# Optimization experiments

Measured on AMD Instinct MI355X. Metric: run time of the kernel, lower is better.

Reference implementation:

```python
import jax, jax.numpy as jnp
import numpy as np

B, S, DIM, H = 8, 1024, 1024, 16
D = DIM // H  # d_head = 64


def setup_inputs() -> dict:
    key = jax.random.key(0)
    ks = jax.random.split(key, 7)
    scale = 1.0 / np.sqrt(D)  # nn.Linear default init range ~ U(-1/sqrt(in), 1/sqrt(in))
    x = jax.random.normal(ks[0], (B, S, DIM), dtype=jnp.float32)
    Wq = jax.random.uniform(ks[1], (H, D, D), jnp.float32, -scale, scale)
    Wk = jax.random.uniform(ks[2], (H, D, D), jnp.float32, -scale, scale)
    Wv = jax.random.uniform(ks[3], (H, D, D), jnp.float32, -scale, scale)
    bq = jax.random.uniform(ks[4], (H, D), jnp.float32, -scale, scale)
    bk = jax.random.uniform(ks[5], (H, D), jnp.float32, -scale, scale)
    bv = jax.random.uniform(ks[6], (H, D), jnp.float32, -scale, scale)
    return {"x": x, "Wq": Wq, "Wk": Wk, "Wv": Wv, "bq": bq, "bk": bk, "bv": bv}


def reference(x, Wq, Wk, Wv, bq, bk, bv):
    # x: [B,S,DIM] -> split heads: [B,S,H,D] (matches per-head column slicing)
    xh = x.reshape(x.shape[0], x.shape[1], H, D)
    # per-head linear: y = x @ W.T + b  (nn.Linear convention: weight [out,in])
    q = jnp.einsum('bshd,hed->bshe', xh, Wq) + bq  # [B,S,H,D]
    k = jnp.einsum('bshd,hed->bshe', xh, Wk) + bk
    v = jnp.einsum('bshd,hed->bshe', xh, Wv) + bv
    scores = jnp.einsum('bqhd,bkhd->bhqk', q, k) / jnp.sqrt(jnp.float32(D))
    attn = jax.nn.softmax(scores, axis=-1)  # [B,H,S,S]
    out = jnp.einsum('bhqk,bkhd->bqhd', attn, v)  # [B,S,H,D]
    # hstack over heads == merge last two dims back to DIM
    return out.reshape(x.shape[0], x.shape[1], H * D)
```

## Files before the change

kernel.cpp:

```cpp
#include <hip/hip_runtime.h>
#include <hip/hip_bf16.h>

#define BB 8
#define SS 1024
#define HH 16
#define DD 64
#define DIMM 1024
#define NUNITS (BB * HH)
#define UNIT_ELEMS (SS * DD)

typedef __attribute__((ext_vector_type(8))) short short8;
typedef __attribute__((ext_vector_type(4))) float f32x4;

#if __has_builtin(__builtin_amdgcn_exp2f)
#define EXP2F(x) __builtin_amdgcn_exp2f(x)
#else
#define EXP2F(x) exp2f(x)
#endif
#if __has_builtin(__builtin_amdgcn_rcpf)
#define RCPF(x) __builtin_amdgcn_rcpf(x)
#else
#define RCPF(x) (1.0f / (x))
#endif

__device__ inline short f2b(float f) {
    unsigned u = __float_as_uint(f);
    u = (u + 0x7FFFu + ((u >> 16) & 1u)) >> 16;
    return (short)u;
}
__device__ inline unsigned pk2(float lo, float hi) {
    unsigned a = __float_as_uint(lo), b = __float_as_uint(hi);
    a = (a + 0x7FFFu + ((a >> 16) & 1u)) >> 16;
    b = (b + 0x7FFFu + ((b >> 16) & 1u)) & 0xFFFF0000u;
    return a | b;
}

__global__ __launch_bounds__(256) void qkv_proj(
    const float* __restrict__ x, const float* __restrict__ Wq,
    const float* __restrict__ Wk, const float* __restrict__ Wv,
    const float* __restrict__ bqp, const float* __restrict__ bkp,
    const float* __restrict__ bvp,
    short* __restrict__ Qo, short* __restrict__ Ko, short* __restrict__ Vto,
    int unit0)
{
    __shared__ alignas(16) short wsm[3][64][72];
    __shared__ alignas(16) short xs[64][72];
    __shared__ alignas(16) short tr[64][72];

    const int t = threadIdx.x;
    const int bid = blockIdx.x;
    const int stg = bid & 3;
    const int ul = bid >> 2;
    const int unit = unit0 + ul;
    const int h = unit & 15;
    const int b = unit >> 4;

    for (int m = 0; m < 3; ++m) {
        const float* src = ((m == 0) ? Wq : (m == 1) ? Wk : Wv) + h * DD * DD;
        for (int i = 0; i < 4; ++i) {
            int g = t + i * 256;
            int e = g >> 4, c = (g & 15) * 4;
            float4 wv = *reinterpret_cast<const float4*>(src + e * DD + c);
            short4 sv; sv.x = f2b(wv.x); sv.y = f2b(wv.y); sv.z = f2b(wv.z); sv.w = f2b(wv.w);
            *reinterpret_cast<short4*>(&wsm[m][e][c]) = sv;
        }
    }

    const int lane = t & 63, w = t >> 6;
    const int l15 = lane & 15, quad = lane >> 4;

    for (int st2 = 0; st2 < 4; ++st2) {
        const int s0 = (stg * 4 + st2) * 64;
        if (st2) __syncthreads();
        for (int i = 0; i < 4; ++i) {
            int g = t + i * 256;
            int r = g >> 4, c = (g & 15) * 4;
            float4 xv = *reinterpret_cast<const float4*>(
                x + ((size_t)(b * SS + s0 + r)) * DIMM + h * DD + c);
            short4 sv; sv.x = f2b(xv.x); sv.y = f2b(xv.y); sv.z = f2b(xv.z); sv.w = f2b(xv.w);
            *reinterpret_cast<short4*>(&xs[r][c]) = sv;
        }
        __syncthreads();

        short8 a0 = *reinterpret_cast<const short8*>(&xs[w * 16 + l15][quad * 8]);
        short8 a1 = *reinterpret_cast<const short8*>(&xs[w * 16 + l15][32 + quad * 8]);

        f32x4 acc[12];
        for (int m = 0; m < 3; ++m)
            for (int et = 0; et < 4; ++et) {
                short8 w0 = *reinterpret_cast<const short8*>(&wsm[m][et * 16 + l15][quad * 8]);
                short8 w1 = *reinterpret_cast<const short8*>(&wsm[m][et * 16 + l15][32 + quad * 8]);
                f32x4 a = {0.f, 0.f, 0.f, 0.f};
                a = __builtin_amdgcn_mfma_f32_16x16x32_bf16(a0, w0, a, 0, 0, 0);
                a = __builtin_amdgcn_mfma_f32_16x16x32_bf16(a1, w1, a, 0, 0, 0);
                acc[m * 4 + et] = a;
            }

        for (int m = 0; m < 3; ++m) {
            if (m) __syncthreads();
            const float* bp = (m == 0) ? bqp : (m == 1) ? bkp : bvp;
            const float scale = (m == 0) ? 0.125f : 1.0f;
            for (int et = 0; et < 4; ++et) {
                float bias = bp[h * DD + et * 16 + l15];
                int e = et * 16 + l15;
                for (int r = 0; r < 4; ++r) {
                    float v = (acc[m * 4 + et][r] + bias) * scale;
                    int srow = w * 16 + quad * 4 + r;
                    if (m == 2) tr[e][srow] = f2b(v);
                    else        tr[srow][e] = f2b(v);
                }
            }
            __syncthreads();
            for (int i = 0; i < 2; ++i) {
                int g = t + i * 256;
                int row = g >> 3, col = (g & 7) * 8;
                short8 val = *reinterpret_cast<const short8*>(&tr[row][col]);
                if (m == 0)
                    *reinterpret_cast<short8*>(Qo + ((size_t)ul * SS + s0 + row) * DD + col) = val;
                else if (m == 1)
                    *reinterpret_cast<short8*>(Ko + ((size_t)ul * SS + s0 + row) * DD + col) = val;
                else
                    *reinterpret_cast<short8*>(Vto + ((size_t)ul * DD + row) * SS + s0 + col) = val;
            }
        }
    }
}

__global__ __launch_bounds__(256, 4) void attn(
    const short* __restrict__ Q, const short* __restrict__ K,
    const short* __restrict__ Vt, float* __restrict__ out, int unit0, int nu)
{
    __shared__ alignas(16) short ks[64][72];
    __shared__ alignas(16) short vts[64][72];
    __shared__ alignas(16) short ps[4][32][72];

    const int t = threadIdx.x;
    const int bid = blockIdx.x;
    int ul, qt;
    if (nu == NUNITS) {
        int xslot = bid & 7;
        int j = bid >> 3;
        ul = xslot * 16 + (j & 15);
        qt = j >> 4;
    } else {
        ul = bid >> 3;
        qt = bid & 7;
    }
    const int unit = unit0 + ul;
    const int h = unit & 15;
    const int b = unit >> 4;
    const int q0 = qt * 128;
    const int lane = t & 63, w = t >> 6;
    const int l15 = lane & 15, quad = lane >> 4;

    short8 qa[2][2];
    for (int s = 0; s < 2; ++s) {
        const short* qp = Q + ((size_t)ul * SS + q0 + s * 64 + w * 16 + l15) * DD;
        qa[s][0] = *reinterpret_cast<const short8*>(qp + quad * 8);
        qa[s][1] = *reinterpret_cast<const short8*>(qp + 32 + quad * 8);
    }

    short8 ones;
    for (int j = 0; j < 8; ++j) ones[j] = (short)0x3F80;

    f32x4 o[8];
    f32x4 lacc[2];
    for (int i = 0; i < 8; ++i) o[i] = (f32x4){0.f, 0.f, 0.f, 0.f};
    lacc[0] = (f32x4){0.f, 0.f, 0.f, 0.f};
    lacc[1] = (f32x4){0.f, 0.f, 0.f, 0.f};

    const int srow_ = t >> 3, scol = (t & 7) * 8;

    const short* kg = K + (size_t)ul * UNIT_ELEMS + srow_ * DD + scol;
    const short* vg = Vt + (size_t)ul * UNIT_ELEMS + srow_ * SS + scol;
    char* ksw = (char*)&ks[srow_][scol];
    char* vtw = (char*)&vts[srow_][scol];
    const char* kbp = (const char*)&ks[l15][quad * 8];
    const char* vbp = (const char*)&vts[l15][quad * 8];
    const char* pap = (const char*)&ps[w][l15][quad * 8];
    char* psw = (char*)&ps[w][l15][quad * 4];

    const float L2E = 1.44269504f;
    const float MBIAS = 11.5415603f;

    for (int kt = 0; kt < 16; ++kt) {
        __syncthreads();
        *reinterpret_cast<short8*>(ksw) = *reinterpret_cast<const short8*>(kg);
        *reinterpret_cast<short8*>(ksw + 32 * 144) = *reinterpret_cast<const short8*>(kg + 32 * DD);
        *reinterpret_cast<short8*>(vtw) = *reinterpret_cast<const short8*>(vg);
        *reinterpret_cast<short8*>(vtw + 32 * 144) = *reinterpret_cast<const short8*>(vg + 32 * SS);
        kg += 64 * DD;
        vg += 64;
        __syncthreads();

        for (int n = 0; n < 4; ++n) {
            short8 kb0 = *reinterpret_cast<const short8*>(kbp + n * 2304);
            short8 kb1 = *reinterpret_cast<const short8*>(kbp + n * 2304 + 64);
            for (int s = 0; s < 2; ++s) {
                f32x4 a = {0.f, 0.f, 0.f, 0.f};
                a = __builtin_amdgcn_mfma_f32_16x16x32_bf16(kb0, qa[s][0], a, 0, 0, 0);
                a = __builtin_amdgcn_mfma_f32_16x16x32_bf16(kb1, qa[s][1], a, 0, 0, 0);
                float p0 = EXP2F(fmaf(a[0], L2E, -MBIAS));
                float p1 = EXP2F(fmaf(a[1], L2E, -MBIAS));
                float p2 = EXP2F(fmaf(a[2], L2E, -MBIAS));
                float p3 = EXP2F(fmaf(a[3], L2E, -MBIAS));
                uint2 pk; pk.x = pk2(p0, p1); pk.y = pk2(p2, p3);
                *reinterpret_cast<uint2*>(psw + s * 2304 + n * 32) = pk;
            }
        }

        short8 pa[2][2];
        for (int s = 0; s < 2; ++s) {
            pa[s][0] = *reinterpret_cast<const short8*>(pap + s * 2304);
            pa[s][1] = *reinterpret_cast<const short8*>(pap + s * 2304 + 64);
            lacc[s] = __builtin_amdgcn_mfma_f32_16x16x32_bf16(pa[s][0], ones, lacc[s], 0, 0, 0);
            lacc[s] = __builtin_amdgcn_mfma_f32_16x16x32_bf16(pa[s][1], ones, lacc[s], 0, 0, 0);
        }
        for (int dt = 0; dt < 4; ++dt) {
            short8 vb0 = *reinterpret_cast<const short8*>(vbp + dt * 2304);
            short8 vb1 = *reinterpret_cast<const short8*>(vbp + dt * 2304 + 64);
            for (int s = 0; s < 2; ++s) {
                o[s * 4 + dt] = __builtin_amdgcn_mfma_f32_16x16x32_bf16(pa[s][0], vb0, o[s * 4 + dt], 0, 0, 0);
                o[s * 4 + dt] = __builtin_amdgcn_mfma_f32_16x16x32_bf16(pa[s][1], vb1, o[s * 4 + dt], 0, 0, 0);
            }
        }
    }

    float* outp = out + ((size_t)b * SS + q0 + w * 16 + quad * 4) * DIMM + h * DD + l15;
    for (int s = 0; s < 2; ++s)
        for (int r = 0; r < 4; ++r) {
            float rin = RCPF(lacc[s][r]);
            for (int dt = 0; dt < 4; ++dt)
                outp[(size_t)(s * 64 + r) * DIMM + dt * 16] = o[s * 4 + dt][r] * rin;
        }
}

extern "C" void kernel_launch(void* const* d_in, const int* in_sizes, int n_in,
                              void* d_out, int out_size, void* d_ws, size_t ws_size,
                              hipStream_t stream) {
    const float* x   = (const float*)d_in[0];
    const float* Wq  = (const float*)d_in[1];
    const float* Wk  = (const float*)d_in[2];
    const float* Wv  = (const float*)d_in[3];
    const float* bqp = (const float*)d_in[4];
    const float* bkp = (const float*)d_in[5];
    const float* bvp = (const float*)d_in[6];
    float* out = (float*)d_out;

    const size_t unit_bytes = 3ULL * UNIT_ELEMS * sizeof(short);
    int U = (int)(ws_size / unit_bytes);
    if (U < 1) U = 1;
    if (U > NUNITS) U = NUNITS;

    short* Qw  = (short*)d_ws;
    short* Kw  = Qw + (size_t)U * UNIT_ELEMS;
    short* Vtw = Kw + (size_t)U * UNIT_ELEMS;

    for (int u0 = 0; u0 < NUNITS; u0 += U) {
        int nu = NUNITS - u0 < U ? NUNITS - u0 : U;
        qkv_proj<<<dim3(nu * 4), dim3(256), 0, stream>>>(
            x, Wq, Wk, Wv, bqp, bkp, bvp, Qw, Kw, Vtw, u0);
        attn<<<dim3(nu * 8), dim3(256), 0, stream>>>(Qw, Kw, Vtw, out, u0, nu);
    }
}
```

Baseline: 154.1 us.

## Rewrite attention inner loop with 32x32 MFMA, async LDS double-buffering, register P

Restructures the attention kernel around 32x32x16 MFMAs computing S^T so the exponentiated probabilities stay in registers. They are converted with v_cvt_pk_bf16 and exchanged across half-waves with permlane32_swap, so the per-wave LDS staging of P is gone. K and V tiles are loaded with global_load_lds into double-buffered, XOR-swizzled LDS, which removes one barrier per iteration and overlaps the next tile's load with compute. Row sums move from ones-MFMAs to VALU adds, and s_setprio is raised around the MFMA blocks. The risks are higher register pressure from the f32x16 accumulators, and correctness now depends on the swizzle and the lane permutation mapping.

Result: faster. 149.2 us (-3.2%).

```diff
diff --git a/kernel.cpp b/kernel.cpp
--- a/kernel.cpp
+++ b/kernel.cpp
@@ -11,6 +11,9 @@
 
 typedef __attribute__((ext_vector_type(8))) short short8;
 typedef __attribute__((ext_vector_type(4))) float f32x4;
+typedef __attribute__((ext_vector_type(16))) float f32x16;
+typedef __attribute__((ext_vector_type(2))) unsigned u32x2;
+typedef __attribute__((ext_vector_type(4))) unsigned u32x4;
 
 #if __has_builtin(__builtin_amdgcn_exp2f)
 #define EXP2F(x) __builtin_amdgcn_exp2f(x)
@@ -28,11 +31,18 @@
     u = (u + 0x7FFFu + ((u >> 16) & 1u)) >> 16;
     return (short)u;
 }
-__device__ inline unsigned pk2(float lo, float hi) {
-    unsigned a = __float_as_uint(lo), b = __float_as_uint(hi);
-    a = (a + 0x7FFFu + ((a >> 16) & 1u)) >> 16;
-    b = (b + 0x7FFFu + ((b >> 16) & 1u)) & 0xFFFF0000u;
-    return a | b;
+
+__device__ __forceinline__ unsigned cvtpk_bf16(float lo, float hi) {
+    unsigned r;
+    asm("v_cvt_pk_bf16_f32 %0, %1, %2" : "=v"(r) : "v"(lo), "v"(hi));
+    return r;
+}
+
+__device__ __forceinline__ void gll16(const void* g, void* l) {
+    __builtin_amdgcn_global_load_lds(
+        (const __attribute__((address_space(1))) void*)g,
+        (__attribute__((address_space(3))) void*)l,
+        16, 0, 0);
 }
 
 __global__ __launch_bounds__(256) void qkv_proj(
@@ -130,9 +140,9 @@
     const short* __restrict__ Q, const short* __restrict__ K,
     const short* __restrict__ Vt, float* __restrict__ out, int unit0, int nu)
 {
-    __shared__ alignas(16) short ks[64][72];
-    __shared__ alignas(16) short vts[64][72];
-    __shared__ alignas(16) short ps[4][32][72];
+    __shared__ alignas(16) short ksm[2][64][64];
+    __shared__ alignas(16) short vsm[2][64][64];
+    __shared__ float lsm[4][32];
 
     const int t = threadIdx.x;
     const int bid = blockIdx.x;
@@ -151,88 +161,124 @@
     const int b = unit >> 4;
     const int q0 = qt * 128;
     const int lane = t & 63, w = t >> 6;
-    const int l15 = lane & 15, quad = lane >> 4;
-
-    short8 qa[2][2];
-    for (int s = 0; s < 2; ++s) {
-        const short* qp = Q + ((size_t)ul * SS + q0 + s * 64 + w * 16 + l15) * DD;
-        qa[s][0] = *reinterpret_cast<const short8*>(qp + quad * 8);
-        qa[s][1] = *reinterpret_cast<const short8*>(qp + 32 + quad * 8);
-    }
-
-    short8 ones;
-    for (int j = 0; j < 8; ++j) ones[j] = (short)0x3F80;
-
-    f32x4 o[8];
-    f32x4 lacc[2];
-    for (int i = 0; i < 8; ++i) o[i] = (f32x4){0.f, 0.f, 0.f, 0.f};
-    lacc[0] = (f32x4){0.f, 0.f, 0.f, 0.f};
-    lacc[1] = (f32x4){0.f, 0.f, 0.f, 0.f};
-
-    const int srow_ = t >> 3, scol = (t & 7) * 8;
-
-    const short* kg = K + (size_t)ul * UNIT_ELEMS + srow_ * DD + scol;
-    const short* vg = Vt + (size_t)ul * UNIT_ELEMS + srow_ * SS + scol;
-    char* ksw = (char*)&ks[srow_][scol];
-    char* vtw = (char*)&vts[srow_][scol];
-    const char* kbp = (const char*)&ks[l15][quad * 8];
-    const char* vbp = (const char*)&vts[l15][quad * 8];
-    const char* pap = (const char*)&ps[w][l15][quad * 8];
-    char* psw = (char*)&ps[w][l15][quad * 4];
+    const int r5 = lane & 31;
+    const int hi = lane >> 5;
+    const int l7 = lane & 7;
+    const int hl4 = (hi ^ l7) << 4;
+
+    short8 qb[4];
+    {
+        const short* qp = Q + ((size_t)ul * SS + q0 + w * 32 + r5) * DD + hi * 8;
+#pragma unroll
+        for (int ds = 0; ds < 4; ++ds)
+            qb[ds] = *reinterpret_cast<const short8*>(qp + ds * 16);
+    }
+
+    const int lrow = lane >> 3, lch = (lane & 7) ^ lrow;
+    const short* kg = K + (size_t)ul * UNIT_ELEMS + (size_t)(w * 8 + lrow) * DD + lch * 8;
+    const short* vg = Vt + ((size_t)ul * DD + w * 8 + lrow) * SS + lch * 8;
+
+    const char* kread0 = (const char*)&ksm[0][0][0] + r5 * 128;
+    const char* vread0 = (const char*)&vsm[0][0][0] + r5 * 128;
+
+    f32x16 o0, o1;
+#pragma unroll
+    for (int i = 0; i < 16; ++i) { o0[i] = 0.f; o1[i] = 0.f; }
+    float lsum = 0.f;
 
     const float L2E = 1.44269504f;
     const float MBIAS = 11.5415603f;
 
+    {
+        short* lk = &ksm[0][w * 8][0];
+        short* lv = &vsm[0][w * 8][0];
+        gll16(kg, lk); gll16(kg + 32 * DD, lk + 32 * 64);
+        gll16(vg, lv); gll16(vg + 32 * SS, lv + 32 * 64);
+        kg += 64 * DD; vg += 64;
+    }
+
     for (int kt = 0; kt < 16; ++kt) {
+        const int cur = kt & 1;
         __syncthreads();
-        *reinterpret_cast<short8*>(ksw) = *reinterpret_cast<const short8*>(kg);
-        *reinterpret_cast<short8*>(ksw + 32 * 144) = *reinterpret_cast<const short8*>(kg + 32 * DD);
-        *reinterpret_cast<short8*>(vtw) = *reinterpret_cast<const short8*>(vg);
-        *reinterpret_cast<short8*>(vtw + 32 * 144) = *reinterpret_cast<const short8*>(vg + 32 * SS);
-        kg += 64 * DD;
-        vg += 64;
-        __syncthreads();
-
-        for (int n = 0; n < 4; ++n) {
-            short8 kb0 = *reinterpret_cast<const short8*>(kbp + n * 2304);
-            short8 kb1 = *reinterpret_cast<const short8*>(kbp + n * 2304 + 64);
-            for (int s = 0; s < 2; ++s) {
-                f32x4 a = {0.f, 0.f, 0.f, 0.f};
-                a = __builtin_amdgcn_mfma_f32_16x16x32_bf16(kb0, qa[s][0], a, 0, 0, 0);
-                a = __builtin_amdgcn_mfma_f32_16x16x32_bf16(kb1, qa[s][1], a, 0, 0, 0);
-                float p0 = EXP2F(fmaf(a[0], L2E, -MBIAS));
-                float p1 = EXP2F(fmaf(a[1], L2E, -MBIAS));
-                float p2 = EXP2F(fmaf(a[2], L2E, -MBIAS));
-                float p3 = EXP2F(fmaf(a[3], L2E, -MBIAS));
-                uint2 pk; pk.x = pk2(p0, p1); pk.y = pk2(p2, p3);
-                *reinterpret_cast<uint2*>(psw + s * 2304 + n * 32) = pk;
+
+        if (kt < 15) {
+            const int nxt = cur ^ 1;
+            short* lk = &ksm[nxt][w * 8][0];
+            short* lv = &vsm[nxt][w * 8][0];
+            gll16(kg, lk); gll16(kg + 32 * DD, lk + 32 * 64);
+            gll16(vg, lv); gll16(vg + 32 * SS, lv + 32 * 64);
+            kg += 64 * DD; vg += 64;
+        }
+
+        const char* kb_ = kread0 + cur * 8192;
+        const char* vb_ = vread0 + cur * 8192;
+
+        f32x16 c0, c1;
+#pragma unroll
+        for (int i = 0; i < 16; ++i) { c0[i] = 0.f; c1[i] = 0.f; }
+
+        __builtin_amdgcn_s_setprio(1);
+#pragma unroll
+        for (int ds = 0; ds < 4; ++ds) {
+            short8 ka = *reinterpret_cast<const short8*>(kb_ + ((ds << 5) ^ hl4));
+            short8 kb = *reinterpret_cast<const short8*>(kb_ + 4096 + ((ds << 5) ^ hl4));
+            c0 = __builtin_amdgcn_mfma_f32_32x32x16_bf16(ka, qb[ds], c0, 0, 0, 0);
+            c1 = __builtin_amdgcn_mfma_f32_32x32x16_bf16(kb, qb[ds], c1, 0, 0, 0);
+        }
+        __builtin_amdgcn_s_setprio(0);
+
+#pragma unroll
+        for (int n = 0; n < 2; ++n) {
+            f32x16 c = n ? c1 : c0;
+            float p[16];
+#pragma unroll
+            for (int r = 0; r < 16; ++r)
+                p[r] = EXP2F(fmaf(c[r], L2E, -MBIAS));
+            lsum += ((((p[0] + p[1]) + (p[2] + p[3])) + ((p[4] + p[5]) + (p[6] + p[7])))
+                   + (((p[8] + p[9]) + (p[10] + p[11])) + ((p[12] + p[13]) + (p[14] + p[15]))));
+
+#pragma unroll
+            for (int bb2 = 0; bb2 < 2; ++bb2) {
+                unsigned u0 = cvtpk_bf16(p[8 * bb2 + 0], p[8 * bb2 + 1]);
+                unsigned u1 = cvtpk_bf16(p[8 * bb2 + 2], p[8 * bb2 + 3]);
+                unsigned v0 = cvtpk_bf16(p[8 * bb2 + 4], p[8 * bb2 + 5]);
+                unsigned v1 = cvtpk_bf16(p[8 * bb2 + 6], p[8 * bb2 + 7]);
+                unsigned w0, w1c, w2, w3;
+#if __has_builtin(__builtin_amdgcn_permlane32_swap)
+                u32x2 r0 = __builtin_amdgcn_permlane32_swap(u0, v0, false, false);
+                u32x2 r1 = __builtin_amdgcn_permlane32_swap(u1, v1, false, false);
+                w0 = r0[0]; w2 = r0[1]; w1c = r1[0]; w3 = r1[1];
+#else
+                unsigned u0s = __shfl_xor(u0, 32), v0s = __shfl_xor(v0, 32);
+                unsigned u1s = __shfl_xor(u1, 32), v1s = __shfl_xor(v1, 32);
+                w0 = hi ? v0s : u0;  w2 = hi ? v0 : u0s;
+                w1c = hi ? v1s : u1; w3 = hi ? v1 : u1s;
+#endif
+                u32x4 aw; aw[0] = w0; aw[1] = w1c; aw[2] = w2; aw[3] = w3;
+                short8 af = __builtin_bit_cast(short8, aw);
+
+                const int ks = n * 2 + bb2;
+                short8 va = *reinterpret_cast<const short8*>(vb_ + ((ks << 5) ^ hl4));
+                short8 vb2 = *reinterpret_cast<const short8*>(vb_ + 4096 + ((ks << 5) ^ hl4));
+                __builtin_amdgcn_s_setprio(1);
+                o0 = __builtin_amdgcn_mfma_f32_32x32x16_bf16(af, va, o0, 0, 0, 0);
+                o1 = __builtin_amdgcn_mfma_f32_32x32x16_bf16(af, vb2, o1, 0, 0, 0);
+                __builtin_amdgcn_s_setprio(0);
             }
         }
-
-        short8 pa[2][2];
-        for (int s = 0; s < 2; ++s) {
-            pa[s][0] = *reinterpret_cast<const short8*>(pap + s * 2304);
-            pa[s][1] = *reinterpret_cast<const short8*>(pap + s * 2304 + 64);
-            lacc[s] = __builtin_amdgcn_mfma_f32_16x16x32_bf16(pa[s][0], ones, lacc[s], 0, 0, 0);
-            lacc[s] = __builtin_amdgcn_mfma_f32_16x16x32_bf16(pa[s][1], ones, lacc[s], 0, 0, 0);
-        }
-        for (int dt = 0; dt < 4; ++dt) {
-            short8 vb0 = *reinterpret_cast<const short8*>(vbp + dt * 2304);
-            short8 vb1 = *reinterpret_cast<const short8*>(vbp + dt * 2304 + 64);
-            for (int s = 0; s < 2; ++s) {
-                o[s * 4 + dt] = __builtin_amdgcn_mfma_f32_16x16x32_bf16(pa[s][0], vb0, o[s * 4 + dt], 0, 0, 0);
-                o[s * 4 + dt] = __builtin_amdgcn_mfma_f32_16x16x32_bf16(pa[s][1], vb1, o[s * 4 + dt], 0, 0, 0);
-            }
-        }
-    }
-
-    float* outp = out + ((size_t)b * SS + q0 + w * 16 + quad * 4) * DIMM + h * DD + l15;
-    for (int s = 0; s < 2; ++s)
-        for (int r = 0; r < 4; ++r) {
-            float rin = RCPF(lacc[s][r]);
-            for (int dt = 0; dt < 4; ++dt)
-                outp[(size_t)(s * 64 + r) * DIMM + dt * 16] = o[s * 4 + dt][r] * rin;
-        }
+    }
+
+    float lt = lsum + __shfl_xor(lsum, 32);
+    if (lane < 32) lsm[w][lane] = lt;
+
+#pragma unroll
+    for (int reg = 0; reg < 16; ++reg) {
+        const int row = (reg & 3) + 8 * (reg >> 2) + 4 * hi;
+        float rin = RCPF(lsm[w][row]);
+        float* op = out + ((size_t)(b * SS + q0 + w * 32 + row)) * DIMM + h * DD + r5;
+        op[0]  = o0[reg] * rin;
+        op[32] = o1[reg] * rin;
+    }
 }
 
 extern "C" void kernel_launch(void* const* d_in, const int* in_sizes, int n_in,
```
